# Optimization experiments

Measured on AMD Instinct MI355X. Metric: run time of the kernel, lower is better.

## Reference

```python
import jax, jax.numpy as jnp
import numpy as np

B, S, D, H = 4, 2048, 1024, 16
HD = D // H  # head dim = 64


def setup_inputs() -> dict:
    key = jax.random.key(0)
    ks = jax.random.split(key, 12)
    s = 1.0 / np.sqrt(D)
    return {
        "query": jax.random.normal(ks[0], (B, S, D), jnp.float32),
        "key": jax.random.normal(ks[1], (B, S, D), jnp.float32),
        "value": jax.random.normal(ks[2], (B, S, D), jnp.float32),
        "attention_mask": jnp.zeros((B, S, S), jnp.float32),
        "Wq": jax.random.normal(ks[3], (D, D), jnp.float32) * s,
        "bq": jax.random.normal(ks[4], (D,), jnp.float32) * s,
        "Wk": jax.random.normal(ks[5], (D, D), jnp.float32) * s,
        "bk": jax.random.normal(ks[6], (D,), jnp.float32) * s,
        "Wv": jax.random.normal(ks[7], (D, D), jnp.float32) * s,
        "bv": jax.random.normal(ks[8], (D,), jnp.float32) * s,
        "Wo": jax.random.normal(ks[9], (D, D), jnp.float32) * s,
        "bo": jax.random.normal(ks[10], (D,), jnp.float32) * s,
    }


def reference(query, key, value, attention_mask, Wq, bq, Wk, bk, Wv, bv, Wo, bo):
    # projections (torch Linear: x @ W.T + b)
    q = query @ Wq.T + bq
    k = key @ Wk.T + bk
    v = value @ Wv.T + bv
    # split heads: [B, S, D] -> [B, H, S, HD]
    split = lambda x: x.reshape(B, S, H, HD).transpose(0, 2, 1, 3)
    q, k, v = split(q), split(k), split(v)
    # scores: [B, H, Sq, Sk], scaled and masked (mask broadcast over heads)
    scores = jnp.einsum("bhqd,bhkd->bhqk", q, k) / jnp.sqrt(jnp.asarray(HD, q.dtype))
    scores = scores + attention_mask[:, None, :, :]
    probs = jax.nn.softmax(scores, axis=-1)
    out = jnp.einsum("bhqk,bhkd->bhqd", probs, v)
    # concat heads: [B, H, S, HD] -> [B, S, D]
    out = out.transpose(0, 2, 1, 3).reshape(B, S, D)
    return out @ Wo.T + bo
```

## Files before the change

kernel.cpp:

```cpp
#include <hip/hip_runtime.h>
#include <hip/hip_bf16.h>


typedef float f32x4 __attribute__((ext_vector_type(4)));
typedef float f32x16 __attribute__((ext_vector_type(16)));
typedef short bf16x8 __attribute__((ext_vector_type(8)));

#define LOG2E 1.4426950408889634f

__device__ __forceinline__ void gload_lds16(const void* g, void* l) {
  __builtin_amdgcn_global_load_lds((const __attribute__((address_space(1))) void*)g,
                                   (__attribute__((address_space(3))) void*)l,
                                   16, 0, 0);
}

__device__ __forceinline__ float fast_exp2(float x) {
#if __has_builtin(__builtin_amdgcn_exp2f)
  return __builtin_amdgcn_exp2f(x);
#else
  return exp2f(x);
#endif
}

__device__ __forceinline__ unsigned bf16bits(float x) {
  __hip_bfloat16 h = __float2bfloat16(x);
  return (unsigned)*(unsigned short*)&h;
}

__device__ __forceinline__ void pl32swap(unsigned& a, unsigned& b, int hi) {
#if __has_builtin(__builtin_amdgcn_permlane32_swap)
  typedef unsigned uint2v __attribute__((ext_vector_type(2)));
  uint2v r = __builtin_amdgcn_permlane32_swap(a, b, false, false);
  a = r[0];
  b = r[1];
#else
  unsigned ax = __shfl_xor((int)a, 32);
  unsigned bx = __shfl_xor((int)b, 32);
  unsigned na = hi ? bx : a;
  unsigned nb = hi ? b : ax;
  a = na;
  b = nb;
#endif
}

__device__ __forceinline__ bf16x8 lds_read_swz(const __hip_bfloat16* base, int row, int colByte) {
  int off = row * 128 + (colByte ^ ((row & 7) << 4));
  return *(const bf16x8*)((const char*)base + off);
}

__global__ __launch_bounds__(256) void cvt3(const float* __restrict__ s0,
                                            const float* __restrict__ s1,
                                            const float* __restrict__ s2,
                                            __hip_bfloat16* __restrict__ d0,
                                            __hip_bfloat16* __restrict__ d1,
                                            __hip_bfloat16* __restrict__ d2, int n) {
  const float* s = blockIdx.z == 0 ? s0 : (blockIdx.z == 1 ? s1 : s2);
  __hip_bfloat16* d = blockIdx.z == 0 ? d0 : (blockIdx.z == 1 ? d1 : d2);
  int i = (blockIdx.x * 256 + threadIdx.x) * 8;
  if (i + 8 <= n) {
    float4 x = *(const float4*)(s + i);
    float4 y = *(const float4*)(s + i + 4);
    bf16x8 v;
    __hip_bfloat16* hv = (__hip_bfloat16*)&v;
    hv[0] = __float2bfloat16(x.x); hv[1] = __float2bfloat16(x.y);
    hv[2] = __float2bfloat16(x.z); hv[3] = __float2bfloat16(x.w);
    hv[4] = __float2bfloat16(y.x); hv[5] = __float2bfloat16(y.y);
    hv[6] = __float2bfloat16(y.z); hv[7] = __float2bfloat16(y.w);
    *(bf16x8*)(d + i) = v;
  }
}

__global__ __launch_bounds__(256) void cvt4(const float* __restrict__ s0,
                                            const float* __restrict__ s1,
                                            const float* __restrict__ s2,
                                            const float* __restrict__ s3,
                                            __hip_bfloat16* __restrict__ d0,
                                            __hip_bfloat16* __restrict__ d1,
                                            __hip_bfloat16* __restrict__ d2,
                                            __hip_bfloat16* __restrict__ d3, int n) {
  const float* s = blockIdx.z == 0 ? s0 : (blockIdx.z == 1 ? s1 : (blockIdx.z == 2 ? s2 : s3));
  __hip_bfloat16* d = blockIdx.z == 0 ? d0 : (blockIdx.z == 1 ? d1 : (blockIdx.z == 2 ? d2 : d3));
  int i = (blockIdx.x * 256 + threadIdx.x) * 8;
  if (i + 8 <= n) {
    float4 x = *(const float4*)(s + i);
    float4 y = *(const float4*)(s + i + 4);
    bf16x8 v;
    __hip_bfloat16* hv = (__hip_bfloat16*)&v;
    hv[0] = __float2bfloat16(x.x); hv[1] = __float2bfloat16(x.y);
    hv[2] = __float2bfloat16(x.z); hv[3] = __float2bfloat16(x.w);
    hv[4] = __float2bfloat16(y.x); hv[5] = __float2bfloat16(y.y);
    hv[6] = __float2bfloat16(y.z); hv[7] = __float2bfloat16(y.w);
    *(bf16x8*)(d + i) = v;
  }
}

__global__ __launch_bounds__(256) void maskrow(const float* __restrict__ m,
                                               unsigned char* __restrict__ flags) {
  int row = blockIdx.x * 4 + (threadIdx.x >> 6);
  int l = threadIdx.x & 63;
  const float* r = m + (size_t)row * 2048;
  float v0 = r[0];
  bool eq = true;
#pragma unroll
  for (int i = 0; i < 8; i++) {
    float4 x = *(const float4*)(r + l * 4 + i * 256);
    eq &= (x.x == v0) & (x.y == v0) & (x.z == v0) & (x.w == v0);
  }
  unsigned long long b = __ballot((int)eq);
  if (l == 0) flags[row] = (b == ~0ull) ? 1 : 0;
}

template <int MODE>
__global__ __launch_bounds__(256) void gemm_nt(const __hip_bfloat16* __restrict__ A,
                                               const __hip_bfloat16* __restrict__ W,
                                               const float* __restrict__ bias,
                                               void* __restrict__ out, float scale) {
  extern __shared__ char smem[];
  __hip_bfloat16(*As)[64] = (__hip_bfloat16(*)[64])smem;
  __hip_bfloat16(*Bs)[64] = (__hip_bfloat16(*)[64])(smem + 128 * 64 * 2);

  const int t = threadIdx.x;
  const int w = t >> 6, l = t & 63;
  const int wm = w >> 1, wn = w & 1;
  const int rowbase = blockIdx.y * 128;
  const int colbase = blockIdx.x * 128;
  const int lr = l & 15, lg = l >> 4;
  const int srow = l >> 3, schunk = (l & 7) * 8;

  f32x4 acc[4][4];
#pragma unroll
  for (int m = 0; m < 4; m++)
#pragma unroll
    for (int n = 0; n < 4; n++) acc[m][n] = {0.f, 0.f, 0.f, 0.f};

  for (int kt = 0; kt < 16; ++kt) {
    const int k0 = kt * 64;
#pragma unroll
    for (int i = 0; i < 4; i++) {
      int r = w * 32 + i * 8;
      gload_lds16(A + (size_t)(rowbase + r + srow) * 1024 + k0 + schunk, &As[r][0]);
      gload_lds16(W + (size_t)(colbase + r + srow) * 1024 + k0 + schunk, &Bs[r][0]);
    }
    __syncthreads();
#pragma unroll
    for (int kk = 0; kk < 2; kk++) {
      bf16x8 a[4], b[4];
#pragma unroll
      for (int m = 0; m < 4; m++) a[m] = *(const bf16x8*)&As[wm * 64 + m * 16 + lr][kk * 32 + lg * 8];
#pragma unroll
      for (int n = 0; n < 4; n++) b[n] = *(const bf16x8*)&Bs[wn * 64 + n * 16 + lr][kk * 32 + lg * 8];
#pragma unroll
      for (int m = 0; m < 4; m++)
#pragma unroll
        for (int n = 0; n < 4; n++)
          acc[m][n] = __builtin_amdgcn_mfma_f32_16x16x32_bf16(a[m], b[n], acc[m][n], 0, 0, 0);
    }
    __syncthreads();
  }

  if (MODE == 0 || MODE == 2) {
#pragma unroll
    for (int m = 0; m < 4; m++) {
#pragma unroll
      for (int r = 0; r < 4; r++) {
        int gi = rowbase + wm * 64 + m * 16 + lg * 4 + r;
#pragma unroll
        for (int n = 0; n < 4; n++) {
          int gj = colbase + wn * 64 + n * 16 + lr;
          float v = (acc[m][n][r] + bias[gj]) * scale;
          if (MODE == 0)
            ((__hip_bfloat16*)out)[(size_t)gi * 1024 + gj] = __float2bfloat16(v);
          else
            ((float*)out)[(size_t)gi * 1024 + gj] = v;
        }
      }
    }
  } else {
    __hip_bfloat16* Ts = (__hip_bfloat16*)smem;
#pragma unroll
    for (int m = 0; m < 4; m++)
#pragma unroll
      for (int r = 0; r < 4; r++) {
        int rr = wm * 64 + m * 16 + lg * 4 + r;
#pragma unroll
        for (int n = 0; n < 4; n++) {
          int c = wn * 64 + n * 16 + lr;
          Ts[rr * 130 + c] = __float2bfloat16(acc[m][n][r] + bias[colbase + c]);
        }
      }
    __syncthreads();
    int d = t >> 1, s0 = (t & 1) * 64;
    int gd = colbase + d;
    int h = gd >> 6, hd = gd & 63;
    int gs = rowbase + s0;
    int b = gs >> 11, sl = gs & 2047;
    __hip_bfloat16* dst = (__hip_bfloat16*)out + ((size_t)(b * 16 + h) * 64 + hd) * 2048 + sl;
#pragma unroll
    for (int c8 = 0; c8 < 8; c8++) {
      bf16x8 v;
#pragma unroll
      for (int j = 0; j < 8; j++)
        ((unsigned short*)&v)[j] = ((const unsigned short*)Ts)[(s0 + c8 * 8 + j) * 130 + d];
      *(bf16x8*)(dst + c8 * 8) = v;
    }
  }
}

__global__ __launch_bounds__(256, 4) void attn(const __hip_bfloat16* __restrict__ Q,
                                               const __hip_bfloat16* __restrict__ K,
                                               const __hip_bfloat16* __restrict__ Vt,
                                               const float* __restrict__ mask,
                                               const unsigned char* __restrict__ flags,
                                               __hip_bfloat16* __restrict__ O) {
  __shared__ __hip_bfloat16 Ks[2][64][64];
  __shared__ __hip_bfloat16 Vs[2][64][64];

  const int t = threadIdx.x, w = t >> 6, l = t & 63;
  const int l31 = l & 31, hi = l >> 5;
  int lin = blockIdx.y * 16 + blockIdx.x;
  lin = (lin & 7) * 128 + (lin >> 3);
  const int qt = lin & 15, bh = lin >> 4;
  const int b = bh >> 4, h = bh & 15;
  const int q0 = qt * 128 + w * 32;
  const size_t bS = (size_t)b * 2048;
  const int srow = l >> 3;
  const int swchunk = ((l & 7) * 8) ^ (srow << 3);

#define STAGE(dbuf, ktile)                                                             \
  do {                                                                                 \
    int kb_ = (ktile) * 64;                                                            \
    _Pragma("unroll") for (int i_ = 0; i_ < 2; i_++) {                                 \
      int r_ = w * 16 + i_ * 8;                                                        \
      gload_lds16(K + (bS + kb_ + r_ + srow) * 1024 + h * 64 + swchunk,                \
                  &Ks[dbuf][r_][0]);                                                   \
      gload_lds16(Vt + ((size_t)bh * 64 + r_ + srow) * 2048 + kb_ + swchunk,           \
                  &Vs[dbuf][r_][0]);                                                   \
    }                                                                                  \
  } while (0)

  bf16x8 qf[4];
#pragma unroll
  for (int c = 0; c < 4; c++)
    qf[c] = *(const bf16x8*)(Q + (bS + q0 + l31) * 1024 + h * 64 + c * 16 + hi * 8);

  f32x16 acco[2];
#pragma unroll
  for (int i = 0; i < 16; i++) { acco[0][i] = 0.f; acco[1][i] = 0.f; }
  float m2 = -1e30f, lsum = 0.f;

  const bool need_mask = !__all((int)(flags[bS + q0 + l31] != 0));
  const float* mrowf = mask + (bS + q0 + l31) * 2048;

  STAGE(0, 0);
  __syncthreads();
  int cur = 0;

  for (int kt = 0; kt < 32; ++kt) {
    const int kb = kt * 64;
    if (kt < 31) STAGE(cur ^ 1, kt + 1);

    f32x16 sc[2];
    if (need_mask) {
#pragma unroll
      for (int ks = 0; ks < 2; ks++)
#pragma unroll
        for (int g = 0; g < 4; g++) {
          float4 tmp = *(const float4*)(mrowf + kb + ks * 32 + g * 8 + hi * 4);
          sc[ks][g * 4 + 0] = tmp.x * LOG2E; sc[ks][g * 4 + 1] = tmp.y * LOG2E;
          sc[ks][g * 4 + 2] = tmp.z * LOG2E; sc[ks][g * 4 + 3] = tmp.w * LOG2E;
        }
    } else {
#pragma unroll
      for (int i = 0; i < 16; i++) { sc[0][i] = 0.f; sc[1][i] = 0.f; }
    }

    __builtin_amdgcn_s_setprio(1);
#pragma unroll
    for (int c = 0; c < 4; c++) {
      bf16x8 ka0 = lds_read_swz(&Ks[cur][0][0], l31, c * 32 + hi * 16);
      sc[0] = __builtin_amdgcn_mfma_f32_32x32x16_bf16(ka0, qf[c], sc[0], 0, 0, 0);
      bf16x8 ka1 = lds_read_swz(&Ks[cur][0][0], 32 + l31, c * 32 + hi * 16);
      sc[1] = __builtin_amdgcn_mfma_f32_32x32x16_bf16(ka1, qf[c], sc[1], 0, 0, 0);
    }
    __builtin_amdgcn_s_setprio(0);

    float mx[16];
#pragma unroll
    for (int r = 0; r < 16; r++) mx[r] = fmaxf(sc[0][r], sc[1][r]);
#pragma unroll
    for (int s = 8; s >= 1; s >>= 1)
#pragma unroll
      for (int r = 0; r < s; r++) mx[r] = fmaxf(mx[r], mx[r + s]);
    float tmax = fmaxf(mx[0], __shfl_xor(mx[0], 32));

    if (__any(tmax > m2 + 8.0f)) {
      float mn = fmaxf(m2, tmax);
      float rs = fast_exp2(m2 - mn);
      m2 = mn;
      lsum *= rs;
#pragma unroll
      for (int r = 0; r < 16; r++) {
        float rsr = __shfl(rs, (r & 3) + 8 * (r >> 2) + 4 * hi);
        acco[0][r] *= rsr;
        acco[1][r] *= rsr;
      }
    }

    float ts0 = 0.f, ts1 = 0.f;
    unsigned pk[2][4][2];
#pragma unroll
    for (int ks = 0; ks < 2; ks++)
#pragma unroll
      for (int g = 0; g < 4; g++)
#pragma unroll
        for (int s = 0; s < 2; s++) {
          float p0 = fast_exp2(sc[ks][g * 4 + s * 2] - m2);
          float p1 = fast_exp2(sc[ks][g * 4 + s * 2 + 1] - m2);
          ts0 += p0;
          ts1 += p1;
          pk[ks][g][s] = (bf16bits(p1) << 16) | bf16bits(p0);
        }
    float tsum = ts0 + ts1;
    tsum += __shfl_xor(tsum, 32);
    lsum += tsum;

    __builtin_amdgcn_s_setprio(1);
#pragma unroll
    for (int ks = 0; ks < 2; ks++) {
#pragma unroll
      for (int c16 = 0; c16 < 2; c16++) {
        unsigned x0 = pk[ks][2 * c16][0], y0 = pk[ks][2 * c16 + 1][0];
        unsigned x1 = pk[ks][2 * c16][1], y1 = pk[ks][2 * c16 + 1][1];
        pl32swap(x0, y0, hi);
        pl32swap(x1, y1, hi);
        bf16x8 pa;
        ((unsigned*)&pa)[0] = x0; ((unsigned*)&pa)[1] = x1;
        ((unsigned*)&pa)[2] = y0; ((unsigned*)&pa)[3] = y1;
#pragma unroll
        for (int ds = 0; ds < 2; ds++) {
          bf16x8 vb = lds_read_swz(&Vs[cur][0][0], ds * 32 + l31, ks * 64 + c16 * 32 + hi * 16);
          acco[ds] = __builtin_amdgcn_mfma_f32_32x32x16_bf16(pa, vb, acco[ds], 0, 0, 0);
        }
      }
    }
    __builtin_amdgcn_s_setprio(0);
    __syncthreads();
    cur ^= 1;
  }
#undef STAGE

  float inv = 1.0f / lsum;
#pragma unroll
  for (int r = 0; r < 16; r++) {
    float invr = __shfl(inv, (r & 3) + 8 * (r >> 2) + 4 * hi);
    int q = q0 + (r & 3) + 8 * (r >> 2) + 4 * hi;
#pragma unroll
    for (int ds = 0; ds < 2; ds++)
      O[(bS + q) * 1024 + h * 64 + ds * 32 + l31] = __float2bfloat16(acco[ds][r] * invr);
  }
}

extern "C" void kernel_launch(void* const* d_in, const int* in_sizes, int n_in,
                              void* d_out, int out_size, void* d_ws, size_t ws_size,
                              hipStream_t stream) {
  const float* q = (const float*)d_in[0];
  const float* k = (const float*)d_in[1];
  const float* v = (const float*)d_in[2];
  const float* msk = (const float*)d_in[3];
  const float* Wq = (const float*)d_in[4];
  const float* bq = (const float*)d_in[5];
  const float* Wk = (const float*)d_in[6];
  const float* bk = (const float*)d_in[7];
  const float* Wv = (const float*)d_in[8];
  const float* bv = (const float*)d_in[9];
  const float* Wo = (const float*)d_in[10];
  const float* bo = (const float*)d_in[11];

  char* ws = (char*)d_ws;
  __hip_bfloat16* qin = (__hip_bfloat16*)(ws);
  __hip_bfloat16* kin = (__hip_bfloat16*)(ws + (16u << 20));
  __hip_bfloat16* vin = (__hip_bfloat16*)(ws + (32u << 20));
  __hip_bfloat16* wqb = (__hip_bfloat16*)(ws + (48u << 20));
  __hip_bfloat16* wkb = (__hip_bfloat16*)(ws + (50u << 20));
  __hip_bfloat16* wvb = (__hip_bfloat16*)(ws + (52u << 20));
  __hip_bfloat16* wob = (__hip_bfloat16*)(ws + (54u << 20));
  __hip_bfloat16* vT  = (__hip_bfloat16*)(ws + (56u << 20));
  unsigned char* flags = (unsigned char*)(ws + (72u << 20));
  __hip_bfloat16* kp  = vin;
  __hip_bfloat16* qp  = kin;
  __hip_bfloat16* oat = qin;

  dim3 blk(256);
  size_t smem = 33280;
  const float qscale = 0.125f * LOG2E;

  cvt3<<<dim3(4096, 1, 3), blk, 0, stream>>>(q, k, v, qin, kin, vin, 8388608);
  cvt4<<<dim3(512, 1, 4), blk, 0, stream>>>(Wq, Wk, Wv, Wo, wqb, wkb, wvb, wob, 1048576);
  maskrow<<<dim3(2048), blk, 0, stream>>>(msk, flags);
  gemm_nt<1><<<dim3(8, 64), blk, smem, stream>>>(vin, wvb, bv, vT, 1.0f);
  gemm_nt<0><<<dim3(8, 64), blk, smem, stream>>>(kin, wkb, bk, kp, 1.0f);
  gemm_nt<0><<<dim3(8, 64), blk, smem, stream>>>(qin, wqb, bq, qp, qscale);
  attn<<<dim3(16, 64), blk, 0, stream>>>(qp, kp, vT, msk, flags, oat);
  gemm_nt<2><<<dim3(8, 64), blk, smem, stream>>>(oat, wob, bo, (float*)d_out, 1.0f);
}
```

Before: 272.5 us.

## Compute softmax row sums via MFMA with ones and use packed bf16 convert

Replaces the scalar per-lane accumulation of exponentiated scores with an extra MFMA that multiplies the bf16 probability tile by a ones vector, so row sums land in the same layout as the output accumulator. It also swaps the two separate float-to-bf16 conversions and shift/or packing for a single v_cvt_pk_bf16_f32 instruction. This removes VALU adds, a cross-lane shuffle per tile and the final broadcast shuffle. In exchange it adds one MFMA per PV step and 16 more accumulator registers. The sum is now taken over bf16-rounded probabilities rather than fp32 ones.

```diff
diff --git a/kernel.cpp b/kernel.cpp
--- a/kernel.cpp
+++ b/kernel.cpp
@@ -22,9 +22,10 @@
 #endif
 }
 
-__device__ __forceinline__ unsigned bf16bits(float x) {
-  __hip_bfloat16 h = __float2bfloat16(x);
-  return (unsigned)*(unsigned short*)&h;
+__device__ __forceinline__ unsigned cvt_pk_bf16(float a, float b) {
+  unsigned r;
+  asm("v_cvt_pk_bf16_f32 %0, %1, %2" : "=v"(r) : "v"(a), "v"(b));
+  return r;
 }
 
 __device__ __forceinline__ void pl32swap(unsigned& a, unsigned& b, int hi) {
@@ -243,10 +244,14 @@
   for (int c = 0; c < 4; c++)
     qf[c] = *(const bf16x8*)(Q + (bS + q0 + l31) * 1024 + h * 64 + c * 16 + hi * 8);
 
-  f32x16 acco[2];
-#pragma unroll
-  for (int i = 0; i < 16; i++) { acco[0][i] = 0.f; acco[1][i] = 0.f; }
-  float m2 = -1e30f, lsum = 0.f;
+  bf16x8 vones;
+#pragma unroll
+  for (int j = 0; j < 8; j++) ((unsigned short*)&vones)[j] = 0x3F80;
+
+  f32x16 acco[2], psum;
+#pragma unroll
+  for (int i = 0; i < 16; i++) { acco[0][i] = 0.f; acco[1][i] = 0.f; psum[i] = 0.f; }
+  float m2 = -1e30f;
 
   const bool need_mask = !__all((int)(flags[bS + q0 + l31] != 0));
   const float* mrowf = mask + (bS + q0 + l31) * 2048;
@@ -297,16 +302,15 @@
       float mn = fmaxf(m2, tmax);
       float rs = fast_exp2(m2 - mn);
       m2 = mn;
-      lsum *= rs;
 #pragma unroll
       for (int r = 0; r < 16; r++) {
         float rsr = __shfl(rs, (r & 3) + 8 * (r >> 2) + 4 * hi);
+        psum[r] *= rsr;
         acco[0][r] *= rsr;
         acco[1][r] *= rsr;
       }
     }
 
-    float ts0 = 0.f, ts1 = 0.f;
     unsigned pk[2][4][2];
 #pragma unroll
     for (int ks = 0; ks < 2; ks++)
@@ -316,13 +320,8 @@
         for (int s = 0; s < 2; s++) {
           float p0 = fast_exp2(sc[ks][g * 4 + s * 2] - m2);
           float p1 = fast_exp2(sc[ks][g * 4 + s * 2 + 1] - m2);
-          ts0 += p0;
-          ts1 += p1;
-          pk[ks][g][s] = (bf16bits(p1) << 16) | bf16bits(p0);
+          pk[ks][g][s] = cvt_pk_bf16(p0, p1);
         }
-    float tsum = ts0 + ts1;
-    tsum += __shfl_xor(tsum, 32);
-    lsum += tsum;
 
     __builtin_amdgcn_s_setprio(1);
 #pragma unroll
@@ -336,6 +335,7 @@
         bf16x8 pa;
         ((unsigned*)&pa)[0] = x0; ((unsigned*)&pa)[1] = x1;
         ((unsigned*)&pa)[2] = y0; ((unsigned*)&pa)[3] = y1;
+        psum = __builtin_amdgcn_mfma_f32_32x32x16_bf16(pa, vones, psum, 0, 0, 0);
 #pragma unroll
         for (int ds = 0; ds < 2; ds++) {
           bf16x8 vb = lds_read_swz(&Vs[cur][0][0], ds * 32 + l31, ks * 64 + c16 * 32 + hi * 16);
@@ -349,10 +349,9 @@
   }
 #undef STAGE
 
-  float inv = 1.0f / lsum;
 #pragma unroll
   for (int r = 0; r < 16; r++) {
-    float invr = __shfl(inv, (r & 3) + 8 * (r >> 2) + 4 * hi);
+    float invr = 1.0f / psum[r];
     int q = q0 + (r & 3) + 8 * (r >> 2) + 4 * hi;
 #pragma unroll
     for (int ds = 0; ds < 2; ds++)
```

Measured after the change: 272.9 us. Within noise of the previous version (+0.1%).
